# Optimization experiments

Hardware: AMD Instinct MI355X
Metric: run time of the kernel (lower is better)

Reference implementation:

```python
import jax, jax.numpy as jnp
import numpy as np

N = 100_000   # nodes
E = 1_200_000 # edges
D = 64        # in_dim
H = 64        # hidden_dim
B = 1000      # graphs in batch
C = 10        # num_classes
TOPO = 64     # topo_dim
BN_EPS = 1e-5


def setup_inputs() -> dict:
    key = jax.random.key(0)
    ks = jax.random.split(key, 24)
    x = jax.random.normal(ks[0], (N, D), dtype=jnp.float32)
    edge_index = jax.random.randint(ks[1], (2, E), 0, N, dtype=jnp.int32)
    # sorted graph ids; force last id = B-1 so batch.max()+1 == B (matches torch path)
    batch = jnp.sort(jax.random.randint(ks[2], (N,), 0, B, dtype=jnp.int32)).at[-1].set(B - 1)
    topo = jax.random.normal(ks[3], (B, TOPO), dtype=jnp.float32)
    s = 0.05
    return {
        "x": x, "edge_index": edge_index, "batch": batch, "topo": topo,
        # conv1 MLP: Linear(D,H) -> BN(H) -> ReLU -> Linear(H,H) -> ReLU
        "W1a": jax.random.normal(ks[4], (D, H)) * s, "b1a": jax.random.normal(ks[5], (H,)) * s,
        "g1": 1.0 + jax.random.normal(ks[6], (H,)) * s, "be1": jax.random.normal(ks[7], (H,)) * s,
        "m1": jax.random.normal(ks[8], (H,)) * s, "v1": 0.5 + jax.random.uniform(ks[9], (H,)),
        "W1b": jax.random.normal(ks[10], (H, H)) * s, "b1b": jax.random.normal(ks[11], (H,)) * s,
        # conv2 MLP: Linear(H,H) -> BN(H) -> ReLU
        "W2": jax.random.normal(ks[12], (H, H)) * s, "b2": jax.random.normal(ks[13], (H,)) * s,
        "g2": 1.0 + jax.random.normal(ks[14], (H,)) * s, "be2": jax.random.normal(ks[15], (H,)) * s,
        "m2": jax.random.normal(ks[16], (H,)) * s, "v2": 0.5 + jax.random.uniform(ks[17], (H,)),
        # topo_net: Linear(TOPO,H) -> ReLU
        "Wt": jax.random.normal(ks[18], (TOPO, H)) * s, "bt": jax.random.normal(ks[19], (H,)) * s,
        # classifier: Linear(2H, C)
        "Wc": jax.random.normal(ks[20], (2 * H, C)) * s, "bc": jax.random.normal(ks[21], (C,)) * s,
    }


def _bn_eval(v, g, b, m, var):
    # BatchNorm1d in eval mode: affine with running stats
    return g * (v - m) * jax.lax.rsqrt(var + BN_EPS) + b


def _gin_agg(h, src, dst):
    # GINConv (eps=0): (1+eps)*x_i + sum_{j->i} x_j ; scatter-add over dst
    return h + jax.ops.segment_sum(h[src], dst, num_segments=N)


def reference(x, edge_index, batch, topo,
              W1a, b1a, g1, be1, m1, v1, W1b, b1b,
              W2, b2, g2, be2, m2, v2, Wt, bt, Wc, bc):
    src, dst = edge_index[0], edge_index[1]
    # conv1: MLP(agg(x)) = Lin -> BN -> ReLU -> Lin -> ReLU; outer relu from forward
    h = _gin_agg(x, src, dst)                              # [N, D]
    h = jax.nn.relu(_bn_eval(h @ W1a + b1a, g1, be1, m1, v1))
    h = jax.nn.relu(h @ W1b + b1b)                         # [N, H]
    h = jax.nn.relu(h)                                     # F.relu(conv1(...))
    # dropout(p=0.5) is identity in eval mode
    # conv2: Lin -> BN -> ReLU, then outer relu
    h = _gin_agg(h, src, dst)                              # [N, H]
    h = jax.nn.relu(_bn_eval(h @ W2 + b2, g2, be2, m2, v2))
    h = jax.nn.relu(h)
    # global_add_pool: sum nodes per graph
    x_struct = jax.ops.segment_sum(h, batch, num_segments=B)   # [B, H]
    # topo already [B, TOPO] => all reshape/pad branches are no-ops
    x_topo = jax.nn.relu(topo @ Wt + bt)                   # [B, H]
    combined = jnp.concatenate([x_struct, x_topo], axis=1) # [B, 2H]
    return combined @ Wc + bc                              # [B, C]
```

## Files before the change

kernel.cpp:

```cpp
#include <hip/hip_runtime.h>

#define N_NODES 100000
#define N_EDGES 1200000
#define DIM     64
#define BGRAPHS 1000
#define NCLASS  10
#define BN_EPS  1e-5f

#define NBUCK   256
#define NPB     391
#define MAGIC   10984572u
#define CHUNK   8192
#define NBLK_P  147
#define SCAN_N  (NBUCK * NBLK_P)
#define CAP     8192

typedef __attribute__((ext_vector_type(8))) short   bfx8;
typedef __attribute__((ext_vector_type(4))) float   f32x4;
typedef __attribute__((ext_vector_type(8))) unsigned short u16x8;

__device__ __forceinline__ unsigned short f2bf(float f) {
    unsigned u = __builtin_bit_cast(unsigned, f);
    unsigned r = (u + 0x7FFFu + ((u >> 16) & 1u)) >> 16;
    return (unsigned short)r;
}
__device__ __forceinline__ float bf2f(unsigned short h) {
    unsigned u = ((unsigned)h) << 16;
    return __builtin_bit_cast(float, u);
}

__global__ void convert_kernel(const float* __restrict__ x, unsigned short* __restrict__ xb,
                               float* __restrict__ xs) {
    int i = blockIdx.x * blockDim.x + threadIdx.x;
    const int n8 = N_NODES * DIM / 8;
    if (i < n8) {
        float4 a = ((const float4*)x)[i * 2];
        float4 b = ((const float4*)x)[i * 2 + 1];
        u16x8 o;
        o[0] = f2bf(a.x); o[1] = f2bf(a.y); o[2] = f2bf(a.z); o[3] = f2bf(a.w);
        o[4] = f2bf(b.x); o[5] = f2bf(b.y); o[6] = f2bf(b.z); o[7] = f2bf(b.w);
        ((u16x8*)xb)[i] = o;
    }
    if (i < BGRAPHS * DIM) xs[i] = 0.f;
}

__global__ __launch_bounds__(256) void histA_kernel(const int* __restrict__ ei,
                                                    int* __restrict__ hist) {
    __shared__ int cnt[NBUCK];
    int t = threadIdx.x, blk = blockIdx.x;
    cnt[t] = 0;
    __syncthreads();
    int e0 = blk * CHUNK;
    for (int i = t; i < CHUNK; i += 256) {
        int e = e0 + i;
        if (e >= N_EDGES) break;
        unsigned d = (unsigned)ei[N_EDGES + e];
        int b = __umulhi(d, MAGIC);
        atomicAdd(&cnt[b], 1);
    }
    __syncthreads();
    hist[t * NBLK_P + blk] = cnt[t];
}

__global__ __launch_bounds__(256) void scan1_kernel(const int* __restrict__ in,
                                                    int* __restrict__ outp,
                                                    int* __restrict__ bsum, int n) {
    __shared__ int tmp[256];
    int t = threadIdx.x;
    int base = blockIdx.x * 1024;
    int v[4]; int s = 0;
    #pragma unroll
    for (int j = 0; j < 4; ++j) {
        int idx = base + t * 4 + j;
        v[j] = (idx < n) ? in[idx] : 0;
        s += v[j];
    }
    tmp[t] = s;
    __syncthreads();
    for (int off = 1; off < 256; off <<= 1) {
        int a = (t >= off) ? tmp[t - off] : 0;
        __syncthreads();
        tmp[t] += a;
        __syncthreads();
    }
    int excl = tmp[t] - s;
    if (t == 255) bsum[blockIdx.x] = tmp[255];
    int run = excl;
    #pragma unroll
    for (int j = 0; j < 4; ++j) {
        int idx = base + t * 4 + j;
        if (idx < n) outp[idx] = run;
        run += v[j];
    }
}

__global__ __launch_bounds__(128) void scan2_kernel(int* __restrict__ bsum, int nb) {
    __shared__ int tmp[128];
    int t = threadIdx.x;
    int v = (t < nb) ? bsum[t] : 0;
    tmp[t] = v;
    __syncthreads();
    for (int off = 1; off < 128; off <<= 1) {
        int a = (t >= off) ? tmp[t - off] : 0;
        __syncthreads();
        tmp[t] += a;
        __syncthreads();
    }
    if (t < nb) bsum[t] = tmp[t] - v;
}

__global__ void scan3_kernel(int* __restrict__ arr, const int* __restrict__ bsum, int n) {
    int i = blockIdx.x * blockDim.x + threadIdx.x;
    if (i < n) arr[i] += bsum[i >> 10];
}

__global__ __launch_bounds__(256) void part_kernel(const int* __restrict__ ei,
                                                   const int* __restrict__ base,
                                                   int* __restrict__ srcbuf,
                                                   unsigned short* __restrict__ dstlbuf) {
    __shared__ int cur[NBUCK];
    int t = threadIdx.x, blk = blockIdx.x;
    cur[t] = base[t * NBLK_P + blk];
    __syncthreads();
    int e0 = blk * CHUNK;
    for (int i = t; i < CHUNK; i += 256) {
        int e = e0 + i;
        if (e >= N_EDGES) break;
        unsigned d = (unsigned)ei[N_EDGES + e];
        int s = ei[e];
        int b = __umulhi(d, MAGIC);
        int pos = atomicAdd(&cur[b], 1);
        srcbuf[pos] = s;
        dstlbuf[pos] = (unsigned short)(d - b * NPB);
    }
}

__global__ __launch_bounds__(256) void refine_kernel(const int* __restrict__ srcbuf,
                                                     const unsigned short* __restrict__ dstlbuf,
                                                     const int* __restrict__ base,
                                                     int* __restrict__ csr_src,
                                                     int* __restrict__ rowptr) {
    __shared__ int cnt[NPB + 1];
    __shared__ int cur[NPB + 1];
    __shared__ int tmp[256];
    __shared__ int outb[CAP];
    int t = threadIdx.x, b = blockIdx.x;
    int beg = base[b * NBLK_P];
    int end = (b == NBUCK - 1) ? N_EDGES : base[(b + 1) * NBLK_P];

    for (int i = t; i < NPB + 1; i += 256) cnt[i] = 0;
    __syncthreads();
    for (int i = beg + t; i < end; i += 256)
        atomicAdd(&cnt[dstlbuf[i]], 1);
    __syncthreads();

    int i0 = 2 * t, i1 = 2 * t + 1;
    int v0 = (i0 < NPB) ? cnt[i0] : 0;
    int v1 = (i1 < NPB) ? cnt[i1] : 0;
    int s = v0 + v1;
    tmp[t] = s;
    __syncthreads();
    for (int off = 1; off < 256; off <<= 1) {
        int a = (t >= off) ? tmp[t - off] : 0;
        __syncthreads();
        tmp[t] += a;
        __syncthreads();
    }
    int excl = tmp[t] - s;
    if (i0 < NPB) cur[i0] = excl;
    if (i1 < NPB) cur[i1] = excl + v0;
    {
        int g0 = b * NPB + i0;
        if (i0 < NPB && g0 < N_NODES) rowptr[g0] = beg + excl;
        int g1 = b * NPB + i1;
        if (i1 < NPB && g1 < N_NODES) rowptr[g1] = beg + excl + v0;
    }
    if (b == NBUCK - 1 && t == 0) rowptr[N_NODES] = N_EDGES;
    __syncthreads();

    for (int i = beg + t; i < end; i += 256) {
        int dl = dstlbuf[i];
        int pos = atomicAdd(&cur[dl], 1);
        if (pos < CAP) outb[pos] = srcbuf[i];
    }
    __syncthreads();

    int nb = end - beg; if (nb > CAP) nb = CAP;
    for (int i = t; i < nb; i += 256) csr_src[beg + i] = outb[i];
}

__global__ __launch_bounds__(256) void gather_kernel(const unsigned short* __restrict__ feat,
                                                     const int* __restrict__ rowptr,
                                                     const int* __restrict__ csr_src,
                                                     unsigned short* __restrict__ out) {
    int t = threadIdx.x;
    int node = blockIdx.x * 32 + (t >> 3);
    int q = t & 7;
    if (node >= N_NODES) return;
    const u16x8* f8 = (const u16x8*)feat;
    u16x8 sv = f8[(long long)node * 8 + q];
    float acc[8];
    #pragma unroll
    for (int j = 0; j < 8; ++j) acc[j] = bf2f(sv[j]);
    int beg = rowptr[node], end = rowptr[node + 1];
    int k = beg;
    int sn = (k < end) ? csr_src[k] : 0;
    while (k < end) {
        int sc = sn;
        ++k;
        if (k < end) sn = csr_src[k];
        u16x8 v = f8[(long long)sc * 8 + q];
        #pragma unroll
        for (int j = 0; j < 8; ++j) acc[j] += bf2f(v[j]);
    }
    u16x8 o;
    #pragma unroll
    for (int j = 0; j < 8; ++j) o[j] = f2bf(acc[j]);
    ((u16x8*)out)[(long long)node * 8 + q] = o;
}

__device__ __forceinline__ bfx8 load_wfrag(const float* __restrict__ W, int kt, int q, int col) {
    bfx8 f;
    #pragma unroll
    for (int j = 0; j < 8; ++j)
        f[j] = (short)f2bf(W[(kt * 32 + q * 8 + j) * 64 + col]);
    return f;
}

__global__ __launch_bounds__(256) void mlp1_kernel(
    const unsigned short* __restrict__ h0,
    const float* __restrict__ W1a, const float* __restrict__ b1a,
    const float* __restrict__ g1,  const float* __restrict__ be1,
    const float* __restrict__ m1,  const float* __restrict__ v1,
    const float* __restrict__ W1b, const float* __restrict__ b1b,
    unsigned short* __restrict__ h2) {
    __shared__ unsigned short h1t[4][16 * 72];
    __shared__ unsigned short outt[4][16 * 64];

    int t = threadIdx.x;
    int w = t >> 6, lane = t & 63;
    int m = lane & 15, q = lane >> 4;
    int row0 = blockIdx.x * 64 + w * 16;

    bfx8 wa[4][2], wb[4][2];
    #pragma unroll
    for (int nt = 0; nt < 4; ++nt) {
        #pragma unroll
        for (int kt = 0; kt < 2; ++kt) {
            wa[nt][kt] = load_wfrag(W1a, kt, q, nt * 16 + m);
            wb[nt][kt] = load_wfrag(W1b, kt, q, nt * 16 + m);
        }
    }
    float A1[4], B1[4], B2c[4];
    #pragma unroll
    for (int nt = 0; nt < 4; ++nt) {
        int c = nt * 16 + m;
        float s = g1[c] * rsqrtf(v1[c] + BN_EPS);
        A1[nt] = s;
        B1[nt] = b1a[c] * s + (be1[c] - m1[c] * s);
        B2c[nt] = b1b[c];
    }

    int rowA = row0 + m;
    if (rowA > N_NODES - 1) rowA = N_NODES - 1;
    const bfx8* ap = (const bfx8*)(h0 + (long long)rowA * 64);
    bfx8 a0 = ap[q];
    bfx8 a1 = ap[4 + q];
    f32x4 acc[4];
    #pragma unroll
    for (int nt = 0; nt < 4; ++nt) {
        acc[nt] = (f32x4){0.f, 0.f, 0.f, 0.f};
        acc[nt] = __builtin_amdgcn_mfma_f32_16x16x32_bf16(a0, wa[nt][0], acc[nt], 0, 0, 0);
        acc[nt] = __builtin_amdgcn_mfma_f32_16x16x32_bf16(a1, wa[nt][1], acc[nt], 0, 0, 0);
    }
    #pragma unroll
    for (int nt = 0; nt < 4; ++nt)
        #pragma unroll
        for (int r = 0; r < 4; ++r) {
            float v = fmaxf(acc[nt][r] * A1[nt] + B1[nt], 0.f);
            h1t[w][(q * 4 + r) * 72 + nt * 16 + m] = f2bf(v);
        }
    __syncthreads();

    const bfx8* hp = (const bfx8*)&h1t[w][m * 72];
    bfx8 c0 = hp[q];
    bfx8 c1 = hp[4 + q];
    f32x4 acc2[4];
    #pragma unroll
    for (int nt = 0; nt < 4; ++nt) {
        acc2[nt] = (f32x4){0.f, 0.f, 0.f, 0.f};
        acc2[nt] = __builtin_amdgcn_mfma_f32_16x16x32_bf16(c0, wb[nt][0], acc2[nt], 0, 0, 0);
        acc2[nt] = __builtin_amdgcn_mfma_f32_16x16x32_bf16(c1, wb[nt][1], acc2[nt], 0, 0, 0);
    }
    #pragma unroll
    for (int nt = 0; nt < 4; ++nt)
        #pragma unroll
        for (int r = 0; r < 4; ++r) {
            float v = fmaxf(acc2[nt][r] + B2c[nt], 0.f);
            outt[w][(q * 4 + r) * 64 + nt * 16 + m] = f2bf(v);
        }
    __syncthreads();

    #pragma unroll
    for (int i = lane; i < 128; i += 64) {
        int rr = i >> 3, cc = i & 7;
        int rg = row0 + rr;
        if (rg < N_NODES)
            ((float4*)h2)[(long long)rg * 8 + cc] = *(const float4*)&outt[w][rr * 64 + cc * 8];
    }
}

__global__ __launch_bounds__(256) void mlp2_kernel(
    const unsigned short* __restrict__ h3,
    const float* __restrict__ W2, const float* __restrict__ b2,
    const float* __restrict__ g2, const float* __restrict__ be2,
    const float* __restrict__ m2, const float* __restrict__ v2,
    const int* __restrict__ batch,
    float* __restrict__ xs) {
    __shared__ float pool[64 * 64];
    __shared__ int bts[64];

    int t = threadIdx.x;
    int w = t >> 6, lane = t & 63;
    int m = lane & 15, q = lane >> 4;
    int row0b = blockIdx.x * 64;
    int row0 = row0b + w * 16;

    bfx8 wf[4][2];
    #pragma unroll
    for (int nt = 0; nt < 4; ++nt)
        #pragma unroll
        for (int kt = 0; kt < 2; ++kt)
            wf[nt][kt] = load_wfrag(W2, kt, q, nt * 16 + m);
    float A[4], Bc[4];
    #pragma unroll
    for (int nt = 0; nt < 4; ++nt) {
        int c = nt * 16 + m;
        float s = g2[c] * rsqrtf(v2[c] + BN_EPS);
        A[nt] = s;
        Bc[nt] = b2[c] * s + (be2[c] - m2[c] * s);
    }
    if (t < 64) {
        int rg = row0b + t;
        bts[t] = (rg < N_NODES) ? batch[rg] : -1;
    }

    int rowA = row0 + m;
    if (rowA > N_NODES - 1) rowA = N_NODES - 1;
    const bfx8* ap = (const bfx8*)(h3 + (long long)rowA * 64);
    bfx8 a0 = ap[q];
    bfx8 a1 = ap[4 + q];
    f32x4 acc[4];
    #pragma unroll
    for (int nt = 0; nt < 4; ++nt) {
        acc[nt] = (f32x4){0.f, 0.f, 0.f, 0.f};
        acc[nt] = __builtin_amdgcn_mfma_f32_16x16x32_bf16(a0, wf[nt][0], acc[nt], 0, 0, 0);
        acc[nt] = __builtin_amdgcn_mfma_f32_16x16x32_bf16(a1, wf[nt][1], acc[nt], 0, 0, 0);
    }
    #pragma unroll
    for (int nt = 0; nt < 4; ++nt)
        #pragma unroll
        for (int r = 0; r < 4; ++r) {
            float v = fmaxf(acc[nt][r] * A[nt] + Bc[nt], 0.f);
            pool[(w * 16 + q * 4 + r) * 64 + nt * 16 + m] = v;
        }
    __syncthreads();

    int col = t & 63;
    int r0 = (t >> 6) * 16;
    int cb = bts[r0];
    float cur = 0.f;
    #pragma unroll
    for (int r = 0; r < 16; ++r) {
        int b = bts[r0 + r];
        if (b != cb) {
            if (cb >= 0) unsafeAtomicAdd(&xs[cb * 64 + col], cur);
            cb = b;
            cur = 0.f;
        }
        cur += pool[(r0 + r) * 64 + col];
    }
    if (cb >= 0) unsafeAtomicAdd(&xs[cb * 64 + col], cur);
}

__global__ __launch_bounds__(64) void head_kernel(
    const float* __restrict__ xs, const float* __restrict__ topo,
    const float* __restrict__ Wt, const float* __restrict__ bt,
    const float* __restrict__ Wc, const float* __restrict__ bc,
    float* __restrict__ out) {
    __shared__ float trow[64];
    __shared__ float comb[128];
    int b = blockIdx.x;
    int h = threadIdx.x;
    trow[h] = topo[b * 64 + h];
    __syncthreads();
    float acc = bt[h];
    #pragma unroll
    for (int k = 0; k < 64; ++k) acc += trow[k] * Wt[k * 64 + h];
    comb[h] = xs[b * 64 + h];
    comb[64 + h] = fmaxf(acc, 0.f);
    __syncthreads();
    if (h < NCLASS) {
        float o = bc[h];
        #pragma unroll
        for (int k = 0; k < 128; ++k) o += comb[k] * Wc[k * NCLASS + h];
        out[b * NCLASS + h] = o;
    }
}

extern "C" void kernel_launch(void* const* d_in, const int* in_sizes, int n_in,
                              void* d_out, int out_size, void* d_ws, size_t ws_size,
                              hipStream_t stream) {
    const float* x     = (const float*)d_in[0];
    const int*   ei    = (const int*)d_in[1];
    const int*   batch = (const int*)d_in[2];
    const float* topo  = (const float*)d_in[3];
    const float* W1a   = (const float*)d_in[4];
    const float* b1a   = (const float*)d_in[5];
    const float* g1    = (const float*)d_in[6];
    const float* be1   = (const float*)d_in[7];
    const float* m1    = (const float*)d_in[8];
    const float* v1    = (const float*)d_in[9];
    const float* W1b   = (const float*)d_in[10];
    const float* b1b   = (const float*)d_in[11];
    const float* W2    = (const float*)d_in[12];
    const float* b2    = (const float*)d_in[13];
    const float* g2    = (const float*)d_in[14];
    const float* be2   = (const float*)d_in[15];
    const float* m2    = (const float*)d_in[16];
    const float* v2    = (const float*)d_in[17];
    const float* Wt    = (const float*)d_in[18];
    const float* bt    = (const float*)d_in[19];
    const float* Wc    = (const float*)d_in[20];
    const float* bc    = (const float*)d_in[21];
    float* out = (float*)d_out;

    char* p = (char*)d_ws;
    unsigned short* xbf  = (unsigned short*)p; p += (size_t)N_NODES * DIM * 2;
    unsigned short* bufA = (unsigned short*)p; p += (size_t)N_NODES * DIM * 2;
    unsigned short* bufB = (unsigned short*)p; p += (size_t)N_NODES * DIM * 2;
    float* xs      = (float*)p; p += (size_t)BGRAPHS * DIM * 4;
    int*   rowptr  = (int*)p;   p += (size_t)(N_NODES + 16) * 4;
    int*   histc   = (int*)p;   p += (size_t)SCAN_N * 4;
    int*   base    = (int*)p;   p += (size_t)SCAN_N * 4;
    int*   bsum    = (int*)p;   p += 256 * 4;
    int*   srcbuf  = (int*)p;   p += (size_t)N_EDGES * 4;
    unsigned short* dstlbuf = (unsigned short*)p; p += (size_t)N_EDGES * 2;
    int*   csr_src = (int*)p;

    const int NB_C  = (N_NODES * DIM / 8 + 255) / 256;
    const int NB_S1 = (SCAN_N + 1023) / 1024;
    const int NB_S3 = (SCAN_N + 255) / 256;

    convert_kernel<<<NB_C, 256, 0, stream>>>(x, xbf, xs);
    histA_kernel<<<NBLK_P, 256, 0, stream>>>(ei, histc);
    scan1_kernel<<<NB_S1, 256, 0, stream>>>(histc, base, bsum, SCAN_N);
    scan2_kernel<<<1, 128, 0, stream>>>(bsum, NB_S1);
    scan3_kernel<<<NB_S3, 256, 0, stream>>>(base, bsum, SCAN_N);
    part_kernel<<<NBLK_P, 256, 0, stream>>>(ei, base, srcbuf, dstlbuf);
    refine_kernel<<<NBUCK, 256, 0, stream>>>(srcbuf, dstlbuf, base, csr_src, rowptr);

    gather_kernel<<<(N_NODES + 31) / 32, 256, 0, stream>>>(xbf, rowptr, csr_src, bufA);
    mlp1_kernel<<<(N_NODES + 63) / 64, 256, 0, stream>>>(
        bufA, W1a, b1a, g1, be1, m1, v1, W1b, b1b, bufB);
    gather_kernel<<<(N_NODES + 31) / 32, 256, 0, stream>>>(bufB, rowptr, csr_src, bufA);
    mlp2_kernel<<<(N_NODES + 63) / 64, 256, 0, stream>>>(
        bufA, W2, b2, g2, be2, m2, v2, batch, xs);
    head_kernel<<<BGRAPHS, 64, 0, stream>>>(xs, topo, Wt, bt, Wc, bc, out);
}
```

Baseline: 246.3 us.

## Fuse neighbor gather into MLP kernels and precompute packed bf16 weights

The separate gather kernels are removed. Each MLP kernel now gathers its own rows directly in the MFMA fragment layout, with each lane summing 16 features of one node, so the intermediate aggregated buffer is never written to or read back from global memory. A new prep kernel converts the weights once to bf16 in a column-major fragment-friendly layout and precomputes the BN scale and offset, replacing the per-block strided fp32 weight loads. The trade-off is that gather parallelism per node drops from 8 threads to 4, each doing twice the loads. That may reduce memory-level parallelism during the latency-bound neighbor gathers.

New measurement: 263.0 us. +6.8%, slower.

```diff
diff --git a/kernel.cpp b/kernel.cpp
--- a/kernel.cpp
+++ b/kernel.cpp
@@ -42,6 +42,36 @@
         ((u16x8*)xb)[i] = o;
     }
     if (i < BGRAPHS * DIM) xs[i] = 0.f;
+}
+
+__global__ void prep_kernel(const float* __restrict__ W1a, const float* __restrict__ W1b,
+                            const float* __restrict__ W2,
+                            const float* __restrict__ b1a,
+                            const float* __restrict__ g1, const float* __restrict__ be1,
+                            const float* __restrict__ m1, const float* __restrict__ v1,
+                            const float* __restrict__ b2,
+                            const float* __restrict__ g2, const float* __restrict__ be2,
+                            const float* __restrict__ m2, const float* __restrict__ v2,
+                            unsigned short* __restrict__ wpA, unsigned short* __restrict__ wpB,
+                            unsigned short* __restrict__ wpC,
+                            float* __restrict__ s1, float* __restrict__ o1,
+                            float* __restrict__ s2, float* __restrict__ o2) {
+    int t = blockIdx.x * blockDim.x + threadIdx.x;
+    if (t < 3 * 4096) {
+        int mat = t >> 12, i = t & 4095;
+        int col = i >> 6, k = i & 63;
+        const float* W = (mat == 0) ? W1a : ((mat == 1) ? W1b : W2);
+        unsigned short* wp = (mat == 0) ? wpA : ((mat == 1) ? wpB : wpC);
+        wp[i] = f2bf(W[k * 64 + col]);
+    }
+    if (t < 64) {
+        float s = g1[t] * rsqrtf(v1[t] + BN_EPS);
+        s1[t] = s;
+        o1[t] = b1a[t] * s + (be1[t] - m1[t] * s);
+        float s2v = g2[t] * rsqrtf(v2[t] + BN_EPS);
+        s2[t] = s2v;
+        o2[t] = b2[t] * s2v + (be2[t] - m2[t] * s2v);
+    }
 }
 
 __global__ __launch_bounds__(256) void histA_kernel(const int* __restrict__ ei,
@@ -189,50 +219,42 @@
     for (int i = t; i < nb; i += 256) csr_src[beg + i] = outb[i];
 }
 
-__global__ __launch_bounds__(256) void gather_kernel(const unsigned short* __restrict__ feat,
-                                                     const int* __restrict__ rowptr,
-                                                     const int* __restrict__ csr_src,
-                                                     unsigned short* __restrict__ out) {
-    int t = threadIdx.x;
-    int node = blockIdx.x * 32 + (t >> 3);
-    int q = t & 7;
-    if (node >= N_NODES) return;
+__device__ __forceinline__ void gather_row(const unsigned short* __restrict__ feat,
+                                           const int* __restrict__ rowptr,
+                                           const int* __restrict__ csr_src,
+                                           int r, int q, float* acc) {
     const u16x8* f8 = (const u16x8*)feat;
-    u16x8 sv = f8[(long long)node * 8 + q];
-    float acc[8];
-    #pragma unroll
-    for (int j = 0; j < 8; ++j) acc[j] = bf2f(sv[j]);
-    int beg = rowptr[node], end = rowptr[node + 1];
-    int k = beg;
+    u16x8 v0 = f8[(long long)r * 8 + q];
+    u16x8 v1 = f8[(long long)r * 8 + 4 + q];
+    #pragma unroll
+    for (int j = 0; j < 8; ++j) { acc[j] = bf2f(v0[j]); acc[8 + j] = bf2f(v1[j]); }
+    int k = rowptr[r], end = rowptr[r + 1];
     int sn = (k < end) ? csr_src[k] : 0;
     while (k < end) {
         int sc = sn;
         ++k;
         if (k < end) sn = csr_src[k];
-        u16x8 v = f8[(long long)sc * 8 + q];
+        u16x8 p0 = f8[(long long)sc * 8 + q];
+        u16x8 p1 = f8[(long long)sc * 8 + 4 + q];
         #pragma unroll
-        for (int j = 0; j < 8; ++j) acc[j] += bf2f(v[j]);
-    }
-    u16x8 o;
-    #pragma unroll
-    for (int j = 0; j < 8; ++j) o[j] = f2bf(acc[j]);
-    ((u16x8*)out)[(long long)node * 8 + q] = o;
-}
-
-__device__ __forceinline__ bfx8 load_wfrag(const float* __restrict__ W, int kt, int q, int col) {
-    bfx8 f;
-    #pragma unroll
-    for (int j = 0; j < 8; ++j)
-        f[j] = (short)f2bf(W[(kt * 32 + q * 8 + j) * 64 + col]);
-    return f;
-}
-
-__global__ __launch_bounds__(256) void mlp1_kernel(
-    const unsigned short* __restrict__ h0,
-    const float* __restrict__ W1a, const float* __restrict__ b1a,
-    const float* __restrict__ g1,  const float* __restrict__ be1,
-    const float* __restrict__ m1,  const float* __restrict__ v1,
-    const float* __restrict__ W1b, const float* __restrict__ b1b,
+        for (int j = 0; j < 8; ++j) { acc[j] += bf2f(p0[j]); acc[8 + j] += bf2f(p1[j]); }
+    }
+}
+
+__device__ __forceinline__ void pack_frags(const float* acc, bfx8& a0, bfx8& a1) {
+    #pragma unroll
+    for (int j = 0; j < 8; ++j) {
+        a0[j] = (short)f2bf(acc[j]);
+        a1[j] = (short)f2bf(acc[8 + j]);
+    }
+}
+
+__global__ __launch_bounds__(256) void gmlp1_kernel(
+    const unsigned short* __restrict__ feat,
+    const int* __restrict__ rowptr, const int* __restrict__ csr_src,
+    const unsigned short* __restrict__ wpA, const unsigned short* __restrict__ wpB,
+    const float* __restrict__ s1, const float* __restrict__ o1,
+    const float* __restrict__ b1b,
     unsigned short* __restrict__ h2) {
     __shared__ unsigned short h1t[4][16 * 72];
     __shared__ unsigned short outt[4][16 * 64];
@@ -242,43 +264,40 @@
     int m = lane & 15, q = lane >> 4;
     int row0 = blockIdx.x * 64 + w * 16;
 
-    bfx8 wa[4][2], wb[4][2];
-    #pragma unroll
-    for (int nt = 0; nt < 4; ++nt) {
-        #pragma unroll
-        for (int kt = 0; kt < 2; ++kt) {
-            wa[nt][kt] = load_wfrag(W1a, kt, q, nt * 16 + m);
-            wb[nt][kt] = load_wfrag(W1b, kt, q, nt * 16 + m);
-        }
-    }
+    int r = row0 + m;
+    if (r > N_NODES - 1) r = N_NODES - 1;
+
+    float accg[16];
+    gather_row(feat, rowptr, csr_src, r, q, accg);
+    bfx8 a0, a1;
+    pack_frags(accg, a0, a1);
+
+    const bfx8* wA8 = (const bfx8*)wpA;
+    const bfx8* wB8 = (const bfx8*)wpB;
+
     float A1[4], B1[4], B2c[4];
     #pragma unroll
     for (int nt = 0; nt < 4; ++nt) {
         int c = nt * 16 + m;
-        float s = g1[c] * rsqrtf(v1[c] + BN_EPS);
-        A1[nt] = s;
-        B1[nt] = b1a[c] * s + (be1[c] - m1[c] * s);
+        A1[nt] = s1[c];
+        B1[nt] = o1[c];
         B2c[nt] = b1b[c];
     }
 
-    int rowA = row0 + m;
-    if (rowA > N_NODES - 1) rowA = N_NODES - 1;
-    const bfx8* ap = (const bfx8*)(h0 + (long long)rowA * 64);
-    bfx8 a0 = ap[q];
-    bfx8 a1 = ap[4 + q];
     f32x4 acc[4];
     #pragma unroll
     for (int nt = 0; nt < 4; ++nt) {
+        int cb = (nt * 16 + m) * 8;
         acc[nt] = (f32x4){0.f, 0.f, 0.f, 0.f};
-        acc[nt] = __builtin_amdgcn_mfma_f32_16x16x32_bf16(a0, wa[nt][0], acc[nt], 0, 0, 0);
-        acc[nt] = __builtin_amdgcn_mfma_f32_16x16x32_bf16(a1, wa[nt][1], acc[nt], 0, 0, 0);
+        acc[nt] = __builtin_amdgcn_mfma_f32_16x16x32_bf16(a0, wA8[cb + q], acc[nt], 0, 0, 0);
+        acc[nt] = __builtin_amdgcn_mfma_f32_16x16x32_bf16(a1, wA8[cb + 4 + q], acc[nt], 0, 0, 0);
     }
     #pragma unroll
     for (int nt = 0; nt < 4; ++nt)
         #pragma unroll
-        for (int r = 0; r < 4; ++r) {
-            float v = fmaxf(acc[nt][r] * A1[nt] + B1[nt], 0.f);
-            h1t[w][(q * 4 + r) * 72 + nt * 16 + m] = f2bf(v);
+        for (int rr = 0; rr < 4; ++rr) {
+            float v = fmaxf(acc[nt][rr] * A1[nt] + B1[nt], 0.f);
+            h1t[w][(q * 4 + rr) * 72 + nt * 16 + m] = f2bf(v);
         }
     __syncthreads();
 
@@ -288,16 +307,17 @@
     f32x4 acc2[4];
     #pragma unroll
     for (int nt = 0; nt < 4; ++nt) {
+        int cb = (nt * 16 + m) * 8;
         acc2[nt] = (f32x4){0.f, 0.f, 0.f, 0.f};
-        acc2[nt] = __builtin_amdgcn_mfma_f32_16x16x32_bf16(c0, wb[nt][0], acc2[nt], 0, 0, 0);
-        acc2[nt] = __builtin_amdgcn_mfma_f32_16x16x32_bf16(c1, wb[nt][1], acc2[nt], 0, 0, 0);
+        acc2[nt] = __builtin_amdgcn_mfma_f32_16x16x32_bf16(c0, wB8[cb + q], acc2[nt], 0, 0, 0);
+        acc2[nt] = __builtin_amdgcn_mfma_f32_16x16x32_bf16(c1, wB8[cb + 4 + q], acc2[nt], 0, 0, 0);
     }
     #pragma unroll
     for (int nt = 0; nt < 4; ++nt)
         #pragma unroll
-        for (int r = 0; r < 4; ++r) {
-            float v = fmaxf(acc2[nt][r] + B2c[nt], 0.f);
-            outt[w][(q * 4 + r) * 64 + nt * 16 + m] = f2bf(v);
+        for (int rr = 0; rr < 4; ++rr) {
+            float v = fmaxf(acc2[nt][rr] + B2c[nt], 0.f);
+            outt[w][(q * 4 + rr) * 64 + nt * 16 + m] = f2bf(v);
         }
     __syncthreads();
 
@@ -310,11 +330,11 @@
     }
 }
 
-__global__ __launch_bounds__(256) void mlp2_kernel(
-    const unsigned short* __restrict__ h3,
-    const float* __restrict__ W2, const float* __restrict__ b2,
-    const float* __restrict__ g2, const float* __restrict__ be2,
-    const float* __restrict__ m2, const float* __restrict__ v2,
+__global__ __launch_bounds__(256) void gmlp2_kernel(
+    const unsigned short* __restrict__ feat,
+    const int* __restrict__ rowptr, const int* __restrict__ csr_src,
+    const unsigned short* __restrict__ wpC,
+    const float* __restrict__ s2, const float* __restrict__ o2,
     const int* __restrict__ batch,
     float* __restrict__ xs) {
     __shared__ float pool[64 * 64];
@@ -326,43 +346,42 @@
     int row0b = blockIdx.x * 64;
     int row0 = row0b + w * 16;
 
-    bfx8 wf[4][2];
-    #pragma unroll
-    for (int nt = 0; nt < 4; ++nt)
-        #pragma unroll
-        for (int kt = 0; kt < 2; ++kt)
-            wf[nt][kt] = load_wfrag(W2, kt, q, nt * 16 + m);
-    float A[4], Bc[4];
-    #pragma unroll
-    for (int nt = 0; nt < 4; ++nt) {
-        int c = nt * 16 + m;
-        float s = g2[c] * rsqrtf(v2[c] + BN_EPS);
-        A[nt] = s;
-        Bc[nt] = b2[c] * s + (be2[c] - m2[c] * s);
-    }
     if (t < 64) {
         int rg = row0b + t;
         bts[t] = (rg < N_NODES) ? batch[rg] : -1;
     }
 
-    int rowA = row0 + m;
-    if (rowA > N_NODES - 1) rowA = N_NODES - 1;
-    const bfx8* ap = (const bfx8*)(h3 + (long long)rowA * 64);
-    bfx8 a0 = ap[q];
-    bfx8 a1 = ap[4 + q];
+    int r = row0 + m;
+    if (r > N_NODES - 1) r = N_NODES - 1;
+
+    float accg[16];
+    gather_row(feat, rowptr, csr_src, r, q, accg);
+    bfx8 a0, a1;
+    pack_frags(accg, a0, a1);
+
+    const bfx8* wC8 = (const bfx8*)wpC;
+    float A[4], Bc[4];
+    #pragma unroll
+    for (int nt = 0; nt < 4; ++nt) {
+        int c = nt * 16 + m;
+        A[nt] = s2[c];
+        Bc[nt] = o2[c];
+    }
+
     f32x4 acc[4];
     #pragma unroll
     for (int nt = 0; nt < 4; ++nt) {
+        int cb = (nt * 16 + m) * 8;
         acc[nt] = (f32x4){0.f, 0.f, 0.f, 0.f};
-        acc[nt] = __builtin_amdgcn_mfma_f32_16x16x32_bf16(a0, wf[nt][0], acc[nt], 0, 0, 0);
-        acc[nt] = __builtin_amdgcn_mfma_f32_16x16x32_bf16(a1, wf[nt][1], acc[nt], 0, 0, 0);
+        acc[nt] = __builtin_amdgcn_mfma_f32_16x16x32_bf16(a0, wC8[cb + q], acc[nt], 0, 0, 0);
+        acc[nt] = __builtin_amdgcn_mfma_f32_16x16x32_bf16(a1, wC8[cb + 4 + q], acc[nt], 0, 0, 0);
     }
     #pragma unroll
     for (int nt = 0; nt < 4; ++nt)
         #pragma unroll
-        for (int r = 0; r < 4; ++r) {
-            float v = fmaxf(acc[nt][r] * A[nt] + Bc[nt], 0.f);
-            pool[(w * 16 + q * 4 + r) * 64 + nt * 16 + m] = v;
+        for (int rr = 0; rr < 4; ++rr) {
+            float v = fmaxf(acc[nt][rr] * A[nt] + Bc[nt], 0.f);
+            pool[(w * 16 + q * 4 + rr) * 64 + nt * 16 + m] = v;
         }
     __syncthreads();
 
@@ -371,14 +390,14 @@
     int cb = bts[r0];
     float cur = 0.f;
     #pragma unroll
-    for (int r = 0; r < 16; ++r) {
-        int b = bts[r0 + r];
+    for (int rr = 0; rr < 16; ++rr) {
+        int b = bts[r0 + rr];
         if (b != cb) {
             if (cb >= 0) unsafeAtomicAdd(&xs[cb * 64 + col], cur);
             cb = b;
             cur = 0.f;
         }
-        cur += pool[(r0 + r) * 64 + col];
+        cur += pool[(r0 + rr) * 64 + col];
     }
     if (cb >= 0) unsafeAtomicAdd(&xs[cb * 64 + col], cur);
 }
@@ -437,7 +456,6 @@
 
     char* p = (char*)d_ws;
     unsigned short* xbf  = (unsigned short*)p; p += (size_t)N_NODES * DIM * 2;
-    unsigned short* bufA = (unsigned short*)p; p += (size_t)N_NODES * DIM * 2;
     unsigned short* bufB = (unsigned short*)p; p += (size_t)N_NODES * DIM * 2;
     float* xs      = (float*)p; p += (size_t)BGRAPHS * DIM * 4;
     int*   rowptr  = (int*)p;   p += (size_t)(N_NODES + 16) * 4;
@@ -446,13 +464,23 @@
     int*   bsum    = (int*)p;   p += 256 * 4;
     int*   srcbuf  = (int*)p;   p += (size_t)N_EDGES * 4;
     unsigned short* dstlbuf = (unsigned short*)p; p += (size_t)N_EDGES * 2;
-    int*   csr_src = (int*)p;
+    int*   csr_src = (int*)p;   p += (size_t)N_EDGES * 4;
+    unsigned short* wpA = (unsigned short*)p; p += 4096 * 2;
+    unsigned short* wpB = (unsigned short*)p; p += 4096 * 2;
+    unsigned short* wpC = (unsigned short*)p; p += 4096 * 2;
+    float* s1 = (float*)p; p += 64 * 4;
+    float* o1 = (float*)p; p += 64 * 4;
+    float* s2 = (float*)p; p += 64 * 4;
+    float* o2 = (float*)p; p += 64 * 4;
 
     const int NB_C  = (N_NODES * DIM / 8 + 255) / 256;
     const int NB_S1 = (SCAN_N + 1023) / 1024;
     const int NB_S3 = (SCAN_N + 255) / 256;
 
     convert_kernel<<<NB_C, 256, 0, stream>>>(x, xbf, xs);
+    prep_kernel<<<48, 256, 0, stream>>>(W1a, W1b, W2, b1a, g1, be1, m1, v1,
+                                        b2, g2, be2, m2, v2,
+                                        wpA, wpB, wpC, s1, o1, s2, o2);
     histA_kernel<<<NBLK_P, 256, 0, stream>>>(ei, histc);
     scan1_kernel<<<NB_S1, 256, 0, stream>>>(histc, base, bsum, SCAN_N);
     scan2_kernel<<<1, 128, 0, stream>>>(bsum, NB_S1);
@@ -460,11 +488,9 @@
     part_kernel<<<NBLK_P, 256, 0, stream>>>(ei, base, srcbuf, dstlbuf);
     refine_kernel<<<NBUCK, 256, 0, stream>>>(srcbuf, dstlbuf, base, csr_src, rowptr);
 
-    gather_kernel<<<(N_NODES + 31) / 32, 256, 0, stream>>>(xbf, rowptr, csr_src, bufA);
-    mlp1_kernel<<<(N_NODES + 63) / 64, 256, 0, stream>>>(
-        bufA, W1a, b1a, g1, be1, m1, v1, W1b, b1b, bufB);
-    gather_kernel<<<(N_NODES + 31) / 32, 256, 0, stream>>>(bufB, rowptr, csr_src, bufA);
-    mlp2_kernel<<<(N_NODES + 63) / 64, 256, 0, stream>>>(
-        bufA, W2, b2, g2, be2, m2, v2, batch, xs);
+    gmlp1_kernel<<<(N_NODES + 63) / 64, 256, 0, stream>>>(
+        xbf, rowptr, csr_src, wpA, wpB, s1, o1, b1b, bufB);
+    gmlp2_kernel<<<(N_NODES + 63) / 64, 256, 0, stream>>>(
+        bufB, rowptr, csr_src, wpC, s2, o2, batch, xs);
     head_kernel<<<BGRAPHS, 64, 0, stream>>>(xs, topo, Wt, bt, Wc, bc, out);
 }
```
